# Performance work log

Hardware: AMD Instinct MI355X
Metric: run time of the kernel (lower is better)

## Reference

```python
import jax, jax.numpy as jnp
import numpy as np

TEMPERATURE = 0.07
EPS = 1e-6  # arccosh domain clamp: argument must be >= 1


def setup_inputs() -> dict:
    key = jax.random.key(0)
    k1, k2 = jax.random.split(key)
    N, D = 8192, 768
    v_hyp = jax.random.normal(k1, (N, D), dtype=jnp.float32)
    t_hyp = jax.random.normal(k2, (N, D), dtype=jnp.float32)
    c = jnp.float32(1.0)  # curvature (positive scalar)
    return {"v_hyp": v_hyp, "t_hyp": t_hyp, "c": c}


def _pairwise_hyperbolic_dist(v, t, c):
    # Lorentz/hyperboloid pairwise distance with curvature c:
    #   x_time = sqrt(1/c + ||x||^2)
    #   <x,y>_L = x . y - x_time * y_time
    #   d(x,y) = (1/sqrt(c)) * arccosh(clamp(-c * <x,y>_L, min=1+eps))
    inv_c = 1.0 / c
    v_time = jnp.sqrt(inv_c + jnp.sum(v * v, axis=-1))  # [N]
    t_time = jnp.sqrt(inv_c + jnp.sum(t * t, axis=-1))  # [N]
    lorentz = jnp.einsum("nd,md->nm", v, t) - v_time[:, None] * t_time[None, :]
    arg = jnp.maximum(-c * lorentz, 1.0 + EPS)
    return jnp.sqrt(inv_c) * jnp.arccosh(arg)  # [N, N]


def _ce_diag(logits):
    # cross-entropy with labels = arange(N), mean reduction
    logp = jax.nn.log_softmax(logits, axis=-1)
    return -jnp.mean(jnp.diagonal(logp))


def reference(v_hyp, t_hyp, c):
    dist = _pairwise_hyperbolic_dist(v_hyp, t_hyp, c)
    logits = -dist / TEMPERATURE  # [N, N]
    loss_v2t = _ce_diag(logits)
    loss_t2v = _ce_diag(logits.T)
    return (loss_v2t + loss_t2v) * 0.5
```

## Files before the change

kernel.cpp:

```cpp
#include <hip/hip_runtime.h>
#include <hip/hip_bf16.h>
#include <math.h>

#define NROWS 8192
#define DDIM  768
#define TEMP_INV 14.285714285714286f
#define EPSX 1e-6f
#define NKT  12
#define SHIFT 55.0f
#define QS   20.0f
#define SLOT 24576

typedef __attribute__((ext_vector_type(4))) int   i32x4;
typedef unsigned int   u32;

#define GLOAD16(gaddr, laddr)                                                   \
  __builtin_amdgcn_global_load_lds(                                             \
      (const __attribute__((address_space(1))) u32*)(gaddr),                    \
      (__attribute__((address_space(3))) u32*)(laddr), 16, 0, 0)

#define MFMAI8(a,b,c) __builtin_amdgcn_mfma_i32_16x16x64_i8((a),(b),(c),0,0,0)

__device__ __forceinline__ int q8(float x){
  int q = __float2int_rn(x * QS);
  q = q < -127 ? -127 : (q > 127 ? 127 : q);
  return q & 255;
}

__global__ __launch_bounds__(256) void prep_kernel(
    const float* __restrict__ v, const float* __restrict__ t, const float* __restrict__ cptr,
    u32* __restrict__ vb, u32* __restrict__ tb,
    float* __restrict__ vtime, float* __restrict__ ttime, float* __restrict__ diag)
{
  int row = blockIdx.x;
  int tid = threadIdx.x;
  float inv_c = 1.0f / cptr[0];
  const float4* vr = (const float4*)(v + (size_t)row * DDIM);
  const float4* tr = (const float4*)(t + (size_t)row * DDIM);
  u32* vbr = vb + (size_t)row * (DDIM/4);
  u32* tbr = tb + (size_t)row * (DDIM/4);
  float sv = 0.f, st = 0.f, dd = 0.f;
  for (int k = tid; k < DDIM/4; k += 256){
    float4 a = vr[k], b = tr[k];
    sv += a.x*a.x + a.y*a.y + a.z*a.z + a.w*a.w;
    st += b.x*b.x + b.y*b.y + b.z*b.z + b.w*b.w;
    dd += a.x*b.x + a.y*b.y + a.z*b.z + a.w*b.w;
    vbr[k] = (u32)q8(a.x) | ((u32)q8(a.y)<<8) | ((u32)q8(a.z)<<16) | ((u32)q8(a.w)<<24);
    tbr[k] = (u32)q8(b.x) | ((u32)q8(b.y)<<8) | ((u32)q8(b.z)<<16) | ((u32)q8(b.w)<<24);
  }
  for (int o = 32; o; o >>= 1){
    sv += __shfl_down(sv, o);
    st += __shfl_down(st, o);
    dd += __shfl_down(dd, o);
  }
  __shared__ float red[3][4];
  int lane = tid & 63, wid = tid >> 6;
  if (!lane){ red[0][wid]=sv; red[1][wid]=st; red[2][wid]=dd; }
  __syncthreads();
  if (!tid){
    float SV = red[0][0]+red[0][1]+red[0][2]+red[0][3];
    float ST = red[1][0]+red[1][1]+red[1][2]+red[1][3];
    float DD = red[2][0]+red[2][1]+red[2][2]+red[2][3];
    vtime[row] = sqrtf(inv_c + SV);
    ttime[row] = sqrtf(inv_c + ST);
    diag[row]  = DD;
  }
}

__global__ __launch_bounds__(512, 4) void tile_kernel(
    const char* __restrict__ vb, const char* __restrict__ tb,
    const float* __restrict__ vtime, const float* __restrict__ ttime,
    const float* __restrict__ cptr,
    float* __restrict__ rowPsum, float* __restrict__ colPsum)
{
  __shared__ char SMc[3*SLOT];
  __shared__ float vtl2[128], ttl[256];

  const int tid = threadIdx.x;
  const int lane = tid & 63, wid = tid >> 6;
  const int wm = wid >> 2, wn = wid & 3;
  const int lo = lane & 15, hi = lane >> 4;

  const float c = cptr[0];
  const float c2 = c + c;
  const float slog = -(1.0f/sqrtf(c)) * TEMP_INV;
  const float wmin = c2 * (1.0f + EPSX);
  const float kq   = c2 * (1.0f/(QS*QS));

  const int linear = blockIdx.x;
  const int xcd = linear & 7, s = linear >> 3;
  const int xr = xcd & 1, xc = xcd >> 1;
  const int by = xr*32 + (s & 3) + ((s >> 5) << 2);
  const int bx = xc*8 + ((s >> 2) & 7);

  if (tid < 128) vtl2[tid] = c2 * vtime[by*128 + tid];
  if (tid < 256) ttl[tid]  = ttime[bx*256 + tid];

  const char* Abase = vb + (size_t)(by*128) * DDIM;
  const char* Bbase = tb + (size_t)(bx*256) * DDIM;

  const int sx = (tid >> 3) & 3;
  const char* pA  = Abase + (size_t)(tid >> 2)*DDIM        + ((tid & 3) ^ sx)*16;
  const char* pB0 = Bbase + (size_t)(tid >> 2)*DDIM        + ((tid & 3) ^ sx)*16;
  const char* pB1 = Bbase + (size_t)(128 + (tid >> 2))*DDIM + ((tid & 3) ^ sx)*16;
  const int dA  = wid*1024;
  const int dB0 = 8192 + wid*1024;
  const int dB1 = 16384 + wid*1024;

  const int swb  = (hi ^ ((lo >> 1) & 3)) * 16;
  const int arow = (wm*64 + lo) * 64 + swb;
  const int brow = 8192 + (wn*64 + lo) * 64 + swb;

  i32x4 acc[4][4];
  #pragma unroll
  for (int m = 0; m < 4; m++)
    #pragma unroll
    for (int n = 0; n < 4; n++)
      acc[m][n] = (i32x4){0,0,0,0};

#define STG(kt) do{                                                              \
    char* s_ = SMc + ((kt) % 3) * SLOT;                                          \
    GLOAD16(pA  + (kt)*64, s_ + dA);                                             \
    GLOAD16(pB0 + (kt)*64, s_ + dB0);                                            \
    GLOAD16(pB1 + (kt)*64, s_ + dB1); }while(0)

  STG(0); STG(1);
  asm volatile("s_waitcnt vmcnt(3) lgkmcnt(0)" ::: "memory");
  __builtin_amdgcn_s_barrier();

  #pragma unroll
  for (int t = 0; t < NKT; t++){
    const char* S = SMc + (t % 3) * SLOT;
    if (t + 2 < NKT) STG(t + 2);
    i32x4 b[4];
    #pragma unroll
    for (int n = 0; n < 4; n++) b[n] = *(const i32x4*)(S + brow + n*1024);
    i32x4 a0 = *(const i32x4*)(S + arow);
    i32x4 a1 = *(const i32x4*)(S + arow + 1024);
    i32x4 a2 = *(const i32x4*)(S + arow + 2048);
    i32x4 a3 = *(const i32x4*)(S + arow + 3072);
    asm volatile("s_waitcnt lgkmcnt(0)" ::: "memory");
    __builtin_amdgcn_sched_barrier(0);
    __builtin_amdgcn_s_setprio(1);
    #pragma unroll
    for (int n = 0; n < 4; n++){
      acc[0][n] = MFMAI8(a0, b[n], acc[0][n]);
      acc[1][n] = MFMAI8(a1, b[n], acc[1][n]);
      acc[2][n] = MFMAI8(a2, b[n], acc[2][n]);
      acc[3][n] = MFMAI8(a3, b[n], acc[3][n]);
    }
    __builtin_amdgcn_s_setprio(0);
    if (t < NKT-2)       asm volatile("s_waitcnt vmcnt(3)" ::: "memory");
    else if (t == NKT-2) asm volatile("s_waitcnt vmcnt(0)" ::: "memory");
    __builtin_amdgcn_s_barrier();
  }
#undef STG

  __syncthreads();

  #pragma unroll
  for (int m = 0; m < 4; m++){
    #pragma unroll
    for (int n = 0; n < 4; n++){
      #pragma unroll
      for (int q = 0; q < 4; q++){
        int r  = wm*64 + m*16 + hi*4 + q;
        int cc = wn*64 + n*16 + lo;
        float w = fmaf(-kq, (float)acc[m][n][q], vtl2[r] * ttl[cc]);
        w = fmaxf(w, wmin);
        acc[m][n][q] = __float_as_int(__expf(fmaf(slog, __logf(w), SHIFT)));
      }
    }
  }

  float* reds  = (float*)SMc;
  float* redcs = reds + 512;

  #pragma unroll
  for (int m = 0; m < 4; m++){
    #pragma unroll
    for (int q = 0; q < 4; q++){
      float s2 = (__int_as_float(acc[m][0][q]) + __int_as_float(acc[m][1][q]))
               + (__int_as_float(acc[m][2][q]) + __int_as_float(acc[m][3][q]));
      #pragma unroll
      for (int msk = 1; msk < 16; msk <<= 1) s2 += __shfl_xor(s2, msk);
      if (lo == 0)
        reds[wn*128 + wm*64 + m*16 + hi*4 + q] = s2;
    }
  }
  __syncthreads();
  if (tid < 128){
    float S = (reds[tid] + reds[128 + tid]) + (reds[256 + tid] + reds[384 + tid]);
    rowPsum[(size_t)bx*NROWS + by*128 + tid] = S;
  }

  #pragma unroll
  for (int n = 0; n < 4; n++){
    float s2 = 0.f;
    #pragma unroll
    for (int m = 0; m < 4; m++)
      #pragma unroll
      for (int q = 0; q < 4; q++) s2 += __int_as_float(acc[m][n][q]);
    s2 += __shfl_xor(s2, 16);
    s2 += __shfl_xor(s2, 32);
    if (hi == 0)
      redcs[wm*256 + wn*64 + n*16 + lo] = s2;
  }
  __syncthreads();
  if (tid < 256){
    float S = redcs[tid] + redcs[256 + tid];
    colPsum[(size_t)by*NROWS + bx*256 + tid] = S;
  }
}

__global__ __launch_bounds__(256) void lse_reduce(
    const float* __restrict__ rowPsum, const float* __restrict__ colPsum,
    float* __restrict__ psums)
{
  const int i = blockIdx.x * 256 + threadIdx.x;
  const float* Ps = blockIdx.y ? colPsum : rowPsum;
  const int nb = blockIdx.y ? 64 : 32;
  float S = 0.f;
  for (int b = 0; b < nb; b++)
    S += Ps[(size_t)b*NROWS + i];
  float lse = __logf(S) - SHIFT;
  for (int o = 32; o; o >>= 1) lse += __shfl_down(lse, o);
  __shared__ float red[4];
  int lane = threadIdx.x & 63, wid = threadIdx.x >> 6;
  if (!lane) red[wid] = lse;
  __syncthreads();
  if (!threadIdx.x)
    psums[blockIdx.y*32 + blockIdx.x] = red[0]+red[1]+red[2]+red[3];
}

__global__ __launch_bounds__(256) void final_kernel(
    const float* __restrict__ psums, const float* __restrict__ vtime,
    const float* __restrict__ ttime, const float* __restrict__ diag,
    const float* __restrict__ cptr, float* __restrict__ out)
{
  int tid = threadIdx.x;
  float c = cptr[0];
  float slog = -(1.0f/sqrtf(c)) * TEMP_INV;
  float dsum = 0.f;
  for (int i = tid; i < NROWS; i += 256){
    float arg = c * (vtime[i]*ttime[i] - diag[i]);
    arg = fmaxf(arg, 1.0f + EPSX);
    dsum += slog * __logf(arg + sqrtf(arg*arg - 1.0f));
  }
  for (int o = 32; o; o >>= 1) dsum += __shfl_down(dsum, o);
  __shared__ float red[4];
  if (!(tid & 63)) red[tid >> 6] = dsum;
  __syncthreads();
  if (!tid){
    float dtot = red[0]+red[1]+red[2]+red[3];
    float rs = 0.f, cs = 0.f;
    for (int k = 0; k < 32; k++){ rs += psums[k]; cs += psums[32+k]; }
    out[0] = 0.5f*(rs + cs)/NROWS - dtot/NROWS;
  }
}

extern "C" void kernel_launch(void* const* d_in, const int* in_sizes, int n_in,
                              void* d_out, int out_size, void* d_ws, size_t ws_size,
                              hipStream_t stream) {
  const float* v = (const float*)d_in[0];
  const float* t = (const float*)d_in[1];
  const float* c = (const float*)d_in[2];

  char* ws = (char*)d_ws;
  const size_t NB = (size_t)NROWS * DDIM;
  char*  vb      = ws;
  char*  tb      = ws + NB;
  float* vtime   = (float*)(ws + 2*NB);
  float* ttime   = (float*)(ws + 2*NB + NROWS*4);
  float* diag    = (float*)(ws + 2*NB + 2*(size_t)NROWS*4);
  char*  p       = ws + 2*NB + 3*(size_t)NROWS*4;
  float* rowPsum = (float*)(p);
  float* colPsum = (float*)(p + (size_t)32*NROWS*4);
  float* psums   = (float*)(p + (size_t)96*NROWS*4);

  prep_kernel<<<NROWS, 256, 0, stream>>>(v, t, c, (u32*)vb, (u32*)tb, vtime, ttime, diag);
  tile_kernel<<<2048, 512, 0, stream>>>(vb, tb, vtime, ttime, c, rowPsum, colPsum);
  lse_reduce<<<dim3(32, 2), 256, 0, stream>>>(rowPsum, colPsum, psums);
  final_kernel<<<1, 256, 0, stream>>>(psums, vtime, ttime, diag, c, (float*)d_out);
}
```

Measured before the change: 125.8 us.

## Load A fragments directly from global, shrink LDS slot, rework prep and final kernels

```diff
diff --git a/kernel.cpp b/kernel.cpp
--- a/kernel.cpp
+++ b/kernel.cpp
@@ -9,7 +9,7 @@
 #define NKT  12
 #define SHIFT 55.0f
 #define QS   20.0f
-#define SLOT 24576
+#define SLOT 16384
 
 typedef __attribute__((ext_vector_type(4))) int   i32x4;
 typedef unsigned int   u32;
@@ -32,15 +32,17 @@
     u32* __restrict__ vb, u32* __restrict__ tb,
     float* __restrict__ vtime, float* __restrict__ ttime, float* __restrict__ diag)
 {
-  int row = blockIdx.x;
-  int tid = threadIdx.x;
-  float inv_c = 1.0f / cptr[0];
+  const int row  = blockIdx.x * 4 + (threadIdx.x >> 6);
+  const int lane = threadIdx.x & 63;
+  const float inv_c = 1.0f / cptr[0];
   const float4* vr = (const float4*)(v + (size_t)row * DDIM);
   const float4* tr = (const float4*)(t + (size_t)row * DDIM);
   u32* vbr = vb + (size_t)row * (DDIM/4);
   u32* tbr = tb + (size_t)row * (DDIM/4);
   float sv = 0.f, st = 0.f, dd = 0.f;
-  for (int k = tid; k < DDIM/4; k += 256){
+  #pragma unroll
+  for (int it = 0; it < 3; it++){
+    int k = lane + it*64;
     float4 a = vr[k], b = tr[k];
     sv += a.x*a.x + a.y*a.y + a.z*a.z + a.w*a.w;
     st += b.x*b.x + b.y*b.y + b.z*b.z + b.w*b.w;
@@ -48,22 +50,16 @@
     vbr[k] = (u32)q8(a.x) | ((u32)q8(a.y)<<8) | ((u32)q8(a.z)<<16) | ((u32)q8(a.w)<<24);
     tbr[k] = (u32)q8(b.x) | ((u32)q8(b.y)<<8) | ((u32)q8(b.z)<<16) | ((u32)q8(b.w)<<24);
   }
+  #pragma unroll
   for (int o = 32; o; o >>= 1){
     sv += __shfl_down(sv, o);
     st += __shfl_down(st, o);
     dd += __shfl_down(dd, o);
   }
-  __shared__ float red[3][4];
-  int lane = tid & 63, wid = tid >> 6;
-  if (!lane){ red[0][wid]=sv; red[1][wid]=st; red[2][wid]=dd; }
-  __syncthreads();
-  if (!tid){
-    float SV = red[0][0]+red[0][1]+red[0][2]+red[0][3];
-    float ST = red[1][0]+red[1][1]+red[1][2]+red[1][3];
-    float DD = red[2][0]+red[2][1]+red[2][2]+red[2][3];
-    vtime[row] = sqrtf(inv_c + SV);
-    ttime[row] = sqrtf(inv_c + ST);
-    diag[row]  = DD;
+  if (!lane){
+    vtime[row] = sqrtf(inv_c + sv);
+    ttime[row] = sqrtf(inv_c + st);
+    diag[row]  = dd;
   }
 }
 
@@ -99,17 +95,19 @@
   const char* Abase = vb + (size_t)(by*128) * DDIM;
   const char* Bbase = tb + (size_t)(bx*256) * DDIM;
 
+  int aoff[4];
+  #pragma unroll
+  for (int m = 0; m < 4; m++)
+    aoff[m] = (wm*64 + m*16 + lo)*DDIM + hi*16;
+
   const int sx = (tid >> 3) & 3;
-  const char* pA  = Abase + (size_t)(tid >> 2)*DDIM        + ((tid & 3) ^ sx)*16;
-  const char* pB0 = Bbase + (size_t)(tid >> 2)*DDIM        + ((tid & 3) ^ sx)*16;
+  const char* pB0 = Bbase + (size_t)(tid >> 2)*DDIM         + ((tid & 3) ^ sx)*16;
   const char* pB1 = Bbase + (size_t)(128 + (tid >> 2))*DDIM + ((tid & 3) ^ sx)*16;
-  const int dA  = wid*1024;
-  const int dB0 = 8192 + wid*1024;
-  const int dB1 = 16384 + wid*1024;
+  const int dB0 = wid*1024;
+  const int dB1 = 8192 + wid*1024;
 
   const int swb  = (hi ^ ((lo >> 1) & 3)) * 16;
-  const int arow = (wm*64 + lo) * 64 + swb;
-  const int brow = 8192 + (wn*64 + lo) * 64 + swb;
+  const int brow = (wn*64 + lo) * 64 + swb;
 
   i32x4 acc[4][4];
   #pragma unroll
@@ -120,25 +118,24 @@
 
 #define STG(kt) do{                                                              \
     char* s_ = SMc + ((kt) % 3) * SLOT;                                          \
-    GLOAD16(pA  + (kt)*64, s_ + dA);                                             \
     GLOAD16(pB0 + (kt)*64, s_ + dB0);                                            \
     GLOAD16(pB1 + (kt)*64, s_ + dB1); }while(0)
 
   STG(0); STG(1);
-  asm volatile("s_waitcnt vmcnt(3) lgkmcnt(0)" ::: "memory");
+  asm volatile("s_waitcnt vmcnt(2) lgkmcnt(0)" ::: "memory");
   __builtin_amdgcn_s_barrier();
 
   #pragma unroll
   for (int t = 0; t < NKT; t++){
     const char* S = SMc + (t % 3) * SLOT;
+    i32x4 a0 = *(const i32x4*)(Abase + aoff[0] + t*64);
+    i32x4 a1 = *(const i32x4*)(Abase + aoff[1] + t*64);
+    i32x4 a2 = *(const i32x4*)(Abase + aoff[2] + t*64);
+    i32x4 a3 = *(const i32x4*)(Abase + aoff[3] + t*64);
     if (t + 2 < NKT) STG(t + 2);
     i32x4 b[4];
     #pragma unroll
     for (int n = 0; n < 4; n++) b[n] = *(const i32x4*)(S + brow + n*1024);
-    i32x4 a0 = *(const i32x4*)(S + arow);
-    i32x4 a1 = *(const i32x4*)(S + arow + 1024);
-    i32x4 a2 = *(const i32x4*)(S + arow + 2048);
-    i32x4 a3 = *(const i32x4*)(S + arow + 3072);
     asm volatile("s_waitcnt lgkmcnt(0)" ::: "memory");
     __builtin_amdgcn_sched_barrier(0);
     __builtin_amdgcn_s_setprio(1);
@@ -150,7 +147,7 @@
       acc[3][n] = MFMAI8(a3, b[n], acc[3][n]);
     }
     __builtin_amdgcn_s_setprio(0);
-    if (t < NKT-2)       asm volatile("s_waitcnt vmcnt(3)" ::: "memory");
+    if (t < NKT-2)       asm volatile("s_waitcnt vmcnt(2)" ::: "memory");
     else if (t == NKT-2) asm volatile("s_waitcnt vmcnt(0)" ::: "memory");
     __builtin_amdgcn_s_barrier();
   }
@@ -233,7 +230,7 @@
     psums[blockIdx.y*32 + blockIdx.x] = red[0]+red[1]+red[2]+red[3];
 }
 
-__global__ __launch_bounds__(256) void final_kernel(
+__global__ __launch_bounds__(1024) void final_kernel(
     const float* __restrict__ psums, const float* __restrict__ vtime,
     const float* __restrict__ ttime, const float* __restrict__ diag,
     const float* __restrict__ cptr, float* __restrict__ out)
@@ -242,20 +239,26 @@
   float c = cptr[0];
   float slog = -(1.0f/sqrtf(c)) * TEMP_INV;
   float dsum = 0.f;
-  for (int i = tid; i < NROWS; i += 256){
+  #pragma unroll
+  for (int it = 0; it < 8; it++){
+    int i = tid + it*1024;
     float arg = c * (vtime[i]*ttime[i] - diag[i]);
     arg = fmaxf(arg, 1.0f + EPSX);
     dsum += slog * __logf(arg + sqrtf(arg*arg - 1.0f));
   }
   for (int o = 32; o; o >>= 1) dsum += __shfl_down(dsum, o);
-  __shared__ float red[4];
+  __shared__ float red[16];
   if (!(tid & 63)) red[tid >> 6] = dsum;
   __syncthreads();
-  if (!tid){
-    float dtot = red[0]+red[1]+red[2]+red[3];
-    float rs = 0.f, cs = 0.f;
-    for (int k = 0; k < 32; k++){ rs += psums[k]; cs += psums[32+k]; }
-    out[0] = 0.5f*(rs + cs)/NROWS - dtot/NROWS;
+  if (tid < 64){
+    float p = psums[tid];
+    for (int o = 32; o; o >>= 1) p += __shfl_down(p, o);
+    if (!tid){
+      float dtot = 0.f;
+      #pragma unroll
+      for (int k = 0; k < 16; k++) dtot += red[k];
+      out[0] = 0.5f*p/NROWS - dtot/NROWS;
+    }
   }
 }
 
@@ -278,8 +281,8 @@
   float* colPsum = (float*)(p + (size_t)32*NROWS*4);
   float* psums   = (float*)(p + (size_t)96*NROWS*4);
 
-  prep_kernel<<<NROWS, 256, 0, stream>>>(v, t, c, (u32*)vb, (u32*)tb, vtime, ttime, diag);
+  prep_kernel<<<2048, 256, 0, stream>>>(v, t, c, (u32*)vb, (u32*)tb, vtime, ttime, diag);
   tile_kernel<<<2048, 512, 0, stream>>>(vb, tb, vtime, ttime, c, rowPsum, colPsum);
   lse_reduce<<<dim3(32, 2), 256, 0, stream>>>(rowPsum, colPsum, psums);
-  final_kernel<<<1, 256, 0, stream>>>(psums, vtime, ttime, diag, c, (float*)d_out);
-}
+  final_kernel<<<1, 1024, 0, stream>>>(psums, vtime, ttime, diag, c, (float*)d_out);
+}
```

New measurement: 162.0 us. +28.8%, slower.
